# Kernel optimization log

Hardware: AMD Instinct MI355X
Metric: run time of the kernel (lower is better)

Reference implementation:

```python
import jax, jax.numpy as jnp
import numpy as np


def setup_inputs() -> dict:
    key = jax.random.key(0)
    ks = jax.random.split(key, 8)
    B, I, H, O, K = 4096, 512, 512, 512, 16
    s = 0.02
    return {
        "sample": jax.random.normal(ks[0], (B, I), jnp.float32),
        "hiddens": jax.random.normal(ks[1], (K, B, H), jnp.float32),
        "mem_para": jax.random.uniform(ks[2], (B, H), jnp.float32),
        "Wu": jax.random.normal(ks[3], (I + H, H), jnp.float32) * s,
        "bu": jnp.zeros((H,), jnp.float32),
        "Wr": jax.random.normal(ks[4], (I + H, H), jnp.float32) * s,
        "br": jnp.zeros((H,), jnp.float32),
        "Wm": jax.random.normal(ks[5], (I + 2 * H, H), jnp.float32) * s,
        "bm": jnp.zeros((H,), jnp.float32),
        "Wh": jax.random.normal(ks[6], (I + H, H), jnp.float32) * s,
        "bh": jnp.zeros((H,), jnp.float32),
        "Wo": jax.random.normal(ks[7], (H, O), jnp.float32) * s,
        "bo": jnp.zeros((O,), jnp.float32),
    }


def _mem_filter(hiddens, mem_para):
    # hiddens: [k, B, H]; mem_para (memory gate output, 'd'): [B, H]
    # Original per-scalar recurrence: w[k]=1; w[k-1-i] = w[k-i]*(i-d)/(i+1)
    # => w[k-1-i] = cumprod_{m=0..i} (m-d)/(m+1), i.e. signed fractional binomials.
    k = hiddens.shape[0]
    i = jnp.arange(k, dtype=hiddens.dtype)[:, None, None]          # [k,1,1]
    factors = (i - mem_para[None]) / (i + 1.0)                      # [k,B,H]
    weights = jnp.flip(jnp.cumprod(factors, axis=0), axis=0)        # [k,B,H]
    return jnp.sum(hiddens * weights, axis=0)                       # [B,H]


def reference(sample, hiddens, mem_para, Wu, bu, Wr, br, Wm, bm, Wh, bh, Wo, bo):
    hidden = hiddens[-1]                                            # [B,H]
    xh = jnp.concatenate([sample, hidden], axis=1)                  # [B,I+H]
    xhd = jnp.concatenate([xh, mem_para], axis=1)                   # [B,I+2H]
    update_gate = jax.nn.sigmoid(xh @ Wu + bu)
    reset_gate = jax.nn.sigmoid(xh @ Wr + br)
    memory_gate = 0.5 * jax.nn.sigmoid(xhd @ Wm + bm)
    xrh = jnp.concatenate([sample, reset_gate * hidden], axis=1)
    h_tilde = jnp.tanh(xrh @ Wh + bh)
    hiddens_filtered = -_mem_filter(hiddens, memory_gate)
    hidden_now = hiddens_filtered + update_gate * h_tilde           # [B,H]
    updated_hiddens = jnp.concatenate([hiddens[1:], hidden_now[None]], axis=0)
    output = hidden_now @ Wo + bo                                   # [B,O]
    return (output, updated_hiddens, memory_gate)
```

## Files before the change

### kernel.cpp

```cpp
#include <hip/hip_runtime.h>
#include <math.h>

typedef __bf16 bf16;
typedef __bf16 bf16x8 __attribute__((ext_vector_type(8)));
typedef __bf16 bf16x4 __attribute__((ext_vector_type(4)));
typedef float  f32x4  __attribute__((ext_vector_type(4)));

constexpr int BATCH = 4096;
constexpr int HID   = 512;
constexpr int NSTEP = 16;
constexpr int SLICE = BATCH * HID;
constexpr int S4    = SLICE / 4;

__device__ __forceinline__ float sigmoidf_(float x) {
    return 1.0f / (1.0f + __expf(-x));
}
__device__ __forceinline__ float tanh_fast(float x) {
    x = fminf(fmaxf(x, -15.0f), 15.0f);
    float e = __expf(2.0f * x);
    return (e - 1.0f) / (e + 1.0f);
}

__device__ __forceinline__ void gload_lds16(const void* g, void* l) {
    __builtin_amdgcn_global_load_lds((const __attribute__((address_space(1))) void*)g,
                                     (__attribute__((address_space(3))) void*)l,
                                     16, 0, 0);
}

__global__ __launch_bounds__(256)
void prep_all(const float* __restrict__ sample,
              const float* __restrict__ hidden,
              const float* __restrict__ mem_para,
              const float* __restrict__ Wu, const float* __restrict__ Wr,
              const float* __restrict__ Wm, const float* __restrict__ Wh,
              const float* __restrict__ Wo,
              bf16* __restrict__ Sb, bf16* __restrict__ Hb, bf16* __restrict__ Mb,
              bf16* __restrict__ Wall_t, bf16* __restrict__ Wh_t,
              bf16* __restrict__ Wo_t) {
    __shared__ float tile[32][33];
    const int bid = blockIdx.x;
    if (bid < 6144) {
        const int seg = bid >> 11;
        const int i = (bid & 2047) * 256 + threadIdx.x;
        const float* in = (seg == 0) ? sample : (seg == 1) ? hidden : mem_para;
        bf16* out = (seg == 0) ? Sb : (seg == 1) ? Hb : Mb;
        float4 v = ((const float4*)in)[i];
        bf16x4 o = {(bf16)v.x, (bf16)v.y, (bf16)v.z, (bf16)v.w};
        ((bf16x4*)out)[i] = o;
        return;
    }
    const int t = bid - 6144;
    const float* in; bf16* out; int stride, row_off, t2;
    if (t < 512)        { in = Wu; out = Wall_t; stride = 1536; row_off = 0;    t2 = t; }
    else if (t < 1024)  { in = Wr; out = Wall_t; stride = 1536; row_off = 512;  t2 = t - 512; }
    else if (t < 1792)  { in = Wm; out = Wall_t; stride = 1536; row_off = 1024; t2 = t - 1024; }
    else if (t < 2304)  { in = Wh; out = Wh_t;   stride = 1024; row_off = 0;    t2 = t - 1792; }
    else                { in = Wo; out = Wo_t;   stride = 512;  row_off = 0;    t2 = t - 2304; }
    const int r0 = (t2 >> 4) * 32, c0 = (t2 & 15) * 32;
    const int tr = threadIdx.x >> 5;
    const int tc = threadIdx.x & 31;
#pragma unroll
    for (int i = 0; i < 4; ++i)
        tile[tr + i * 8][tc] = in[(size_t)(r0 + tr + i * 8) * 512 + c0 + tc];
    __syncthreads();
#pragma unroll
    for (int i = 0; i < 4; ++i) {
        const int c = tr + i * 8;
        out[(size_t)(row_off + c0 + c) * stride + r0 + tc] = (bf16)tile[tc][c];
    }
}

__global__ __launch_bounds__(256)
void gemm_urm_copy(const bf16* __restrict__ Sb,
                   const bf16* __restrict__ Hb,
                   const bf16* __restrict__ Mb,
                   const bf16* __restrict__ Wall_t,
                   const float* __restrict__ bu,
                   const float* __restrict__ br,
                   const float* __restrict__ bm,
                   bf16* __restrict__ UGb,
                   bf16* __restrict__ RHb,
                   float* __restrict__ out_mg,
                   const float* __restrict__ hiddens,
                   float* __restrict__ out_upd) {
    __shared__ bf16 As[128 * 64];
    __shared__ bf16 Bs[64 * 64];

    const int bid = blockIdx.x;
    const int tid = threadIdx.x;

    if (bid >= 768) {
        const int base = (bid - 768) * 4096 + tid;
        const f32x4* src = ((const f32x4*)hiddens) + S4;
        f32x4* dst = (f32x4*)out_upd;
#pragma unroll
        for (int u = 0; u < 16; ++u) {
            const int f = base + u * 256;
            f32x4 v = __builtin_nontemporal_load(src + f);
            __builtin_nontemporal_store(v, dst + f);
        }
        return;
    }

    const int wid  = tid >> 6;
    const int lane = tid & 63;
    const int wr = wid >> 1, wc = wid & 1;
    const int brow = (bid & 31) * 128;
    const int bcol = (bid >> 5) * 64;

    const bf16* segs[3] = {Sb, Hb, Mb};
    const int nkt = (bcol >= 1024) ? 24 : 16;

    const int s_row  = tid >> 3;
    const int s_chnk = tid & 7;

    f32x4 acc[4][2] = {};

    for (int t = 0; t < nkt; ++t) {
        const int k0 = t * 64;
        const bf16* Aseg = segs[k0 >> 9];
        const int kloc = k0 & 511;

#pragma unroll
        for (int c = 0; c < 4; ++c) {
            const int row = c * 32 + s_row;
            const int sc  = s_chnk ^ (row & 7);
            gload_lds16(Aseg + (size_t)(brow + row) * 512 + kloc + sc * 8,
                        As + (size_t)(c * 256 + (wid << 6)) * 8);
        }
#pragma unroll
        for (int c = 0; c < 2; ++c) {
            const int row = c * 32 + s_row;
            const int sc  = s_chnk ^ (row & 7);
            gload_lds16(Wall_t + (size_t)(bcol + row) * 1536 + k0 + sc * 8,
                        Bs + (size_t)(c * 256 + (wid << 6)) * 8);
        }
        __syncthreads();

#pragma unroll
        for (int ks = 0; ks < 2; ++ks) {
            const int kb = ks * 64 + ((lane >> 4) << 4);
            bf16x8 bfrag[2];
#pragma unroll
            for (int ni = 0; ni < 2; ++ni) {
                const int n = wc * 32 + ni * 16 + (lane & 15);
                bfrag[ni] = *(const bf16x8*)((const char*)Bs +
                                             n * 128 + (kb ^ ((n & 7) << 4)));
            }
#pragma unroll
            for (int mi = 0; mi < 4; ++mi) {
                const int m = wr * 64 + mi * 16 + (lane & 15);
                const bf16x8 afrag = *(const bf16x8*)((const char*)As +
                                                      m * 128 + (kb ^ ((m & 7) << 4)));
#pragma unroll
                for (int ni = 0; ni < 2; ++ni)
                    acc[mi][ni] = __builtin_amdgcn_mfma_f32_16x16x32_bf16(
                        afrag, bfrag[ni], acc[mi][ni], 0, 0, 0);
            }
        }
        __syncthreads();
    }

    const int lr4 = (lane >> 4) * 4;
    const int lc  = lane & 15;
#pragma unroll
    for (int mi = 0; mi < 4; ++mi) {
#pragma unroll
        for (int ni = 0; ni < 2; ++ni) {
            const int col = bcol + wc * 32 + ni * 16 + lc;
            const f32x4 a = acc[mi][ni];
#pragma unroll
            for (int r = 0; r < 4; ++r) {
                const int row = brow + wr * 64 + mi * 16 + lr4 + r;
                const float x = a[r];
                if (col < 512) {
                    UGb[(size_t)row * 512 + col] = (bf16)sigmoidf_(x + bu[col]);
                } else if (col < 1024) {
                    const int c2 = col - 512;
                    const float v = sigmoidf_(x + br[c2]) *
                                    (float)Hb[(size_t)row * 512 + c2];
                    RHb[(size_t)row * 512 + c2] = (bf16)v;
                } else {
                    const int c3 = col - 1024;
                    out_mg[(size_t)row * 512 + c3] = 0.5f * sigmoidf_(x + bm[c3]);
                }
            }
        }
    }
}

__global__ __launch_bounds__(256)
void gemm_wh_sum(const bf16* __restrict__ Sb,
                 const bf16* __restrict__ RHb,
                 const bf16* __restrict__ Wh_t,
                 const float* __restrict__ bh,
                 bf16* __restrict__ HTb,
                 const float* __restrict__ hiddens,
                 const float* __restrict__ mg,
                 float* __restrict__ filt) {
    __shared__ bf16 As[128 * 64];
    __shared__ bf16 Bs[64 * 64];

    const int bid = blockIdx.x;
    const int tid = threadIdx.x;

    if (bid >= 256) {
        const int idx = (bid - 256) * 256 + tid;
        const f32x4 d = ((const f32x4*)mg)[idx];
        f32x4 c = {1.f, 1.f, 1.f, 1.f};
        f32x4 a = {0.f, 0.f, 0.f, 0.f};
#pragma unroll
        for (int i = 0; i < NSTEP; ++i) {
            const int j = NSTEP - 1 - i;
            const f32x4 v = __builtin_nontemporal_load(
                ((const f32x4*)hiddens) + (size_t)j * S4 + idx);
            const float fi = (float)i;
            const float inv = 1.0f / (float)(i + 1);
            c *= (fi - d) * inv;
            a += v * c;
        }
        __builtin_nontemporal_store(a, ((f32x4*)filt) + idx);
        return;
    }

    const int wid  = tid >> 6;
    const int lane = tid & 63;
    const int wr = wid >> 1, wc = wid & 1;
    const int brow = (bid & 31) * 128;
    const int bcol = (bid >> 5) * 64;

    const bf16* segs[2] = {Sb, RHb};

    const int s_row  = tid >> 3;
    const int s_chnk = tid & 7;

    f32x4 acc[4][2] = {};

    for (int t = 0; t < 16; ++t) {
        const int k0 = t * 64;
        const bf16* Aseg = segs[k0 >> 9];
        const int kloc = k0 & 511;

#pragma unroll
        for (int c = 0; c < 4; ++c) {
            const int row = c * 32 + s_row;
            const int sc  = s_chnk ^ (row & 7);
            gload_lds16(Aseg + (size_t)(brow + row) * 512 + kloc + sc * 8,
                        As + (size_t)(c * 256 + (wid << 6)) * 8);
        }
#pragma unroll
        for (int c = 0; c < 2; ++c) {
            const int row = c * 32 + s_row;
            const int sc  = s_chnk ^ (row & 7);
            gload_lds16(Wh_t + (size_t)(bcol + row) * 1024 + k0 + sc * 8,
                        Bs + (size_t)(c * 256 + (wid << 6)) * 8);
        }
        __syncthreads();

#pragma unroll
        for (int ks = 0; ks < 2; ++ks) {
            const int kb = ks * 64 + ((lane >> 4) << 4);
            bf16x8 bfrag[2];
#pragma unroll
            for (int ni = 0; ni < 2; ++ni) {
                const int n = wc * 32 + ni * 16 + (lane & 15);
                bfrag[ni] = *(const bf16x8*)((const char*)Bs +
                                             n * 128 + (kb ^ ((n & 7) << 4)));
            }
#pragma unroll
            for (int mi = 0; mi < 4; ++mi) {
                const int m = wr * 64 + mi * 16 + (lane & 15);
                const bf16x8 afrag = *(const bf16x8*)((const char*)As +
                                                      m * 128 + (kb ^ ((m & 7) << 4)));
#pragma unroll
                for (int ni = 0; ni < 2; ++ni)
                    acc[mi][ni] = __builtin_amdgcn_mfma_f32_16x16x32_bf16(
                        afrag, bfrag[ni], acc[mi][ni], 0, 0, 0);
            }
        }
        __syncthreads();
    }

    const int lr4 = (lane >> 4) * 4;
    const int lc  = lane & 15;
#pragma unroll
    for (int mi = 0; mi < 4; ++mi) {
#pragma unroll
        for (int ni = 0; ni < 2; ++ni) {
            const int col = bcol + wc * 32 + ni * 16 + lc;
            const f32x4 a = acc[mi][ni];
#pragma unroll
            for (int r = 0; r < 4; ++r) {
                const int row = brow + wr * 64 + mi * 16 + lr4 + r;
                HTb[(size_t)row * 512 + col] = (bf16)tanh_fast(a[r] + bh[col]);
            }
        }
    }
}

__global__ __launch_bounds__(256)
void combine(const float* __restrict__ filt,
             const bf16* __restrict__ ugb,
             const bf16* __restrict__ htb,
             float* __restrict__ out_upd,
             bf16* __restrict__ hnb) {
    const int idx = blockIdx.x * 256 + threadIdx.x;
    const f32x4 a = ((const f32x4*)filt)[idx];
    const bf16x4 u = ((const bf16x4*)ugb)[idx];
    const bf16x4 t = ((const bf16x4*)htb)[idx];
    f32x4 hn;
#pragma unroll
    for (int e = 0; e < 4; ++e)
        hn[e] = fmaf((float)u[e], (float)t[e], -a[e]);
    ((f32x4*)out_upd)[(size_t)(NSTEP - 1) * S4 + idx] = hn;
    bf16x4 hb = {(bf16)hn[0], (bf16)hn[1], (bf16)hn[2], (bf16)hn[3]};
    ((bf16x4*)hnb)[idx] = hb;
}

__global__ __launch_bounds__(256)
void gemm_out(const bf16* __restrict__ HNb,
              const bf16* __restrict__ Wo_t,
              const float* __restrict__ bo,
              float* __restrict__ outp) {
    __shared__ bf16 As[128 * 64];
    __shared__ bf16 Bs[64 * 64];

    const int tid  = threadIdx.x;
    const int wid  = tid >> 6;
    const int lane = tid & 63;
    const int wr = wid >> 1, wc = wid & 1;
    const int brow = blockIdx.x * 128;
    const int bcol = blockIdx.y * 64;

    const int s_row  = tid >> 3;
    const int s_chnk = tid & 7;

    f32x4 acc[4][2] = {};

    for (int t = 0; t < 8; ++t) {
        const int k0 = t * 64;

#pragma unroll
        for (int c = 0; c < 4; ++c) {
            const int row = c * 32 + s_row;
            const int sc  = s_chnk ^ (row & 7);
            gload_lds16(HNb + (size_t)(brow + row) * 512 + k0 + sc * 8,
                        As + (size_t)(c * 256 + (wid << 6)) * 8);
        }
#pragma unroll
        for (int c = 0; c < 2; ++c) {
            const int row = c * 32 + s_row;
            const int sc  = s_chnk ^ (row & 7);
            gload_lds16(Wo_t + (size_t)(bcol + row) * 512 + k0 + sc * 8,
                        Bs + (size_t)(c * 256 + (wid << 6)) * 8);
        }
        __syncthreads();

#pragma unroll
        for (int ks = 0; ks < 2; ++ks) {
            const int kb = ks * 64 + ((lane >> 4) << 4);
            bf16x8 bfrag[2];
#pragma unroll
            for (int ni = 0; ni < 2; ++ni) {
                const int n = wc * 32 + ni * 16 + (lane & 15);
                bfrag[ni] = *(const bf16x8*)((const char*)Bs +
                                             n * 128 + (kb ^ ((n & 7) << 4)));
            }
#pragma unroll
            for (int mi = 0; mi < 4; ++mi) {
                const int m = wr * 64 + mi * 16 + (lane & 15);
                const bf16x8 afrag = *(const bf16x8*)((const char*)As +
                                                      m * 128 + (kb ^ ((m & 7) << 4)));
#pragma unroll
                for (int ni = 0; ni < 2; ++ni)
                    acc[mi][ni] = __builtin_amdgcn_mfma_f32_16x16x32_bf16(
                        afrag, bfrag[ni], acc[mi][ni], 0, 0, 0);
            }
        }
        __syncthreads();
    }

    const int lr4 = (lane >> 4) * 4;
    const int lc  = lane & 15;
#pragma unroll
    for (int mi = 0; mi < 4; ++mi) {
#pragma unroll
        for (int ni = 0; ni < 2; ++ni) {
            const int col = bcol + wc * 32 + ni * 16 + lc;
            const f32x4 a = acc[mi][ni];
#pragma unroll
            for (int r = 0; r < 4; ++r) {
                const int row = brow + wr * 64 + mi * 16 + lr4 + r;
                outp[(size_t)row * 512 + col] = a[r] + bo[col];
            }
        }
    }
}

extern "C" void kernel_launch(void* const* d_in, const int* in_sizes, int n_in,
                              void* d_out, int out_size, void* d_ws, size_t ws_size,
                              hipStream_t stream) {
    const float* sample   = (const float*)d_in[0];
    const float* hiddens  = (const float*)d_in[1];
    const float* mem_para = (const float*)d_in[2];
    const float* Wu = (const float*)d_in[3];
    const float* bu = (const float*)d_in[4];
    const float* Wr = (const float*)d_in[5];
    const float* br = (const float*)d_in[6];
    const float* Wm = (const float*)d_in[7];
    const float* bm = (const float*)d_in[8];
    const float* Wh = (const float*)d_in[9];
    const float* bh = (const float*)d_in[10];
    const float* Wo = (const float*)d_in[11];
    const float* bo = (const float*)d_in[12];

    float* out        = (float*)d_out;
    float* out_output = out;
    float* out_upd    = out + SLICE;
    float* out_mg     = out + SLICE + (size_t)NSTEP * SLICE;

    const float* hidden = hiddens + (size_t)(NSTEP - 1) * SLICE;

    char* ws = (char*)d_ws;
    bf16* Sb    = (bf16*)(ws);
    bf16* Hb    = (bf16*)(ws + (((size_t) 4) << 20));
    bf16* Mb    = (bf16*)(ws + (((size_t) 8) << 20));
    bf16* RHb   = (bf16*)(ws + (((size_t)12) << 20));
    bf16* HNb   = (bf16*)(ws + (((size_t)16) << 20));
    bf16* UGb   = (bf16*)(ws + (((size_t)20) << 20));
    bf16* HTb   = (bf16*)(ws + (((size_t)24) << 20));
    bf16* Wall_t = (bf16*)(ws + (((size_t)28) << 20));
    bf16* Wh_t  = (bf16*)(ws + (((size_t)33) << 20));
    bf16* Wo_t  = (bf16*)(ws + (((size_t)35) << 20));
    float* filt = (float*)(ws + (((size_t)40) << 20));

    dim3 blk(256);

    prep_all<<<8704, blk, 0, stream>>>(sample, hidden, mem_para,
                                       Wu, Wr, Wm, Wh, Wo,
                                       Sb, Hb, Mb, Wall_t, Wh_t, Wo_t);
    gemm_urm_copy<<<768 + 1920, blk, 0, stream>>>(
        Sb, Hb, Mb, Wall_t, bu, br, bm, UGb, RHb, out_mg, hiddens, out_upd);
    gemm_wh_sum<<<256 + 2048, blk, 0, stream>>>(
        Sb, RHb, Wh_t, bh, HTb, hiddens, out_mg, filt);
    combine<<<S4 / 256, blk, 0, stream>>>(filt, UGb, HTb, out_upd, HNb);
    gemm_out<<<dim3(32, 8), blk, 0, stream>>>(HNb, Wo_t, bo, out_output);
}
```

Measured before the change: 130.5 us.

## Fuse hiddens shift-copy into filter pass and remap GEMM blocks across XCDs

The separate copy of hiddens[1:] into updated_hiddens is removed from the first GEMM launch. It is now done inside the memory-filter pass, which already reads every hiddens slice, so each slice is read once instead of twice. All three GEMMs also use a new block-index mapping that groups row blocks per XCD (bid&7), with the aim of improving L2 reuse of the A and B tiles. The filter pass switches its loads from nontemporal to normal loads and now issues more stores, which may lengthen that phase.

```diff
diff --git a/kernel.cpp b/kernel.cpp
--- a/kernel.cpp
+++ b/kernel.cpp
@@ -71,45 +71,35 @@
 }
 
 __global__ __launch_bounds__(256)
-void gemm_urm_copy(const bf16* __restrict__ Sb,
-                   const bf16* __restrict__ Hb,
-                   const bf16* __restrict__ Mb,
-                   const bf16* __restrict__ Wall_t,
-                   const float* __restrict__ bu,
-                   const float* __restrict__ br,
-                   const float* __restrict__ bm,
-                   bf16* __restrict__ UGb,
-                   bf16* __restrict__ RHb,
-                   float* __restrict__ out_mg,
-                   const float* __restrict__ hiddens,
-                   float* __restrict__ out_upd) {
+void gemm_urm(const bf16* __restrict__ Sb,
+              const bf16* __restrict__ Hb,
+              const bf16* __restrict__ Mb,
+              const bf16* __restrict__ Wall_t,
+              const float* __restrict__ bu,
+              const float* __restrict__ br,
+              const float* __restrict__ bm,
+              bf16* __restrict__ UGb,
+              bf16* __restrict__ RHb,
+              float* __restrict__ out_mg) {
     __shared__ bf16 As[128 * 64];
     __shared__ bf16 Bs[64 * 64];
 
     const int bid = blockIdx.x;
     const int tid = threadIdx.x;
 
-    if (bid >= 768) {
-        const int base = (bid - 768) * 4096 + tid;
-        const f32x4* src = ((const f32x4*)hiddens) + S4;
-        f32x4* dst = (f32x4*)out_upd;
-#pragma unroll
-        for (int u = 0; u < 16; ++u) {
-            const int f = base + u * 256;
-            f32x4 v = __builtin_nontemporal_load(src + f);
-            __builtin_nontemporal_store(v, dst + f);
-        }
-        return;
-    }
+    const int k8  = bid & 7;
+    const int s   = bid >> 3;
+    const int colb = s >> 2;
+    const int rowb = (k8 << 2) + (s & 3);
+    const int brow = rowb * 128;
+    const int bcol = colb * 64;
 
     const int wid  = tid >> 6;
     const int lane = tid & 63;
     const int wr = wid >> 1, wc = wid & 1;
-    const int brow = (bid & 31) * 128;
-    const int bcol = (bid >> 5) * 64;
 
     const bf16* segs[3] = {Sb, Hb, Mb};
-    const int nkt = (bcol >= 1024) ? 24 : 16;
+    const int nkt = (colb >= 16) ? 24 : 16;
 
     const int s_row  = tid >> 3;
     const int s_chnk = tid & 7;
@@ -190,14 +180,15 @@
 }
 
 __global__ __launch_bounds__(256)
-void gemm_wh_sum(const bf16* __restrict__ Sb,
-                 const bf16* __restrict__ RHb,
-                 const bf16* __restrict__ Wh_t,
-                 const float* __restrict__ bh,
-                 bf16* __restrict__ HTb,
-                 const float* __restrict__ hiddens,
-                 const float* __restrict__ mg,
-                 float* __restrict__ filt) {
+void gemm_wh_filter(const bf16* __restrict__ Sb,
+                    const bf16* __restrict__ RHb,
+                    const bf16* __restrict__ Wh_t,
+                    const float* __restrict__ bh,
+                    bf16* __restrict__ HTb,
+                    const float* __restrict__ hiddens,
+                    const float* __restrict__ mg,
+                    float* __restrict__ out_upd,
+                    float* __restrict__ filt) {
     __shared__ bf16 As[128 * 64];
     __shared__ bf16 Bs[64 * 64];
 
@@ -206,28 +197,36 @@
 
     if (bid >= 256) {
         const int idx = (bid - 256) * 256 + tid;
+        const f32x4* h4 = (const f32x4*)hiddens;
+        f32x4* o4 = (f32x4*)out_upd;
         const f32x4 d = ((const f32x4*)mg)[idx];
         f32x4 c = {1.f, 1.f, 1.f, 1.f};
         f32x4 a = {0.f, 0.f, 0.f, 0.f};
 #pragma unroll
         for (int i = 0; i < NSTEP; ++i) {
             const int j = NSTEP - 1 - i;
-            const f32x4 v = __builtin_nontemporal_load(
-                ((const f32x4*)hiddens) + (size_t)j * S4 + idx);
+            const f32x4 v = h4[(size_t)j * S4 + idx];
             const float fi = (float)i;
             const float inv = 1.0f / (float)(i + 1);
             c *= (fi - d) * inv;
             a += v * c;
-        }
-        __builtin_nontemporal_store(a, ((f32x4*)filt) + idx);
+            if (j >= 1)
+                __builtin_nontemporal_store(v, o4 + (size_t)(j - 1) * S4 + idx);
+        }
+        ((f32x4*)filt)[idx] = a;
         return;
     }
+
+    const int k8  = bid & 7;
+    const int s   = bid >> 3;
+    const int colb = s >> 2;
+    const int rowb = (k8 << 2) + (s & 3);
+    const int brow = rowb * 128;
+    const int bcol = colb * 64;
 
     const int wid  = tid >> 6;
     const int lane = tid & 63;
     const int wr = wid >> 1, wc = wid & 1;
-    const int brow = (bid & 31) * 128;
-    const int bcol = (bid >> 5) * 64;
 
     const bf16* segs[2] = {Sb, RHb};
 
@@ -325,12 +324,19 @@
     __shared__ bf16 As[128 * 64];
     __shared__ bf16 Bs[64 * 64];
 
-    const int tid  = threadIdx.x;
+    const int bid = blockIdx.x;
+    const int tid = threadIdx.x;
+
+    const int k8  = bid & 7;
+    const int s   = bid >> 3;
+    const int colb = s >> 2;
+    const int rowb = (k8 << 2) + (s & 3);
+    const int brow = rowb * 128;
+    const int bcol = colb * 64;
+
     const int wid  = tid >> 6;
     const int lane = tid & 63;
     const int wr = wid >> 1, wc = wid & 1;
-    const int brow = blockIdx.x * 128;
-    const int bcol = blockIdx.y * 64;
 
     const int s_row  = tid >> 3;
     const int s_chnk = tid & 7;
@@ -439,10 +445,10 @@
     prep_all<<<8704, blk, 0, stream>>>(sample, hidden, mem_para,
                                        Wu, Wr, Wm, Wh, Wo,
                                        Sb, Hb, Mb, Wall_t, Wh_t, Wo_t);
-    gemm_urm_copy<<<768 + 1920, blk, 0, stream>>>(
-        Sb, Hb, Mb, Wall_t, bu, br, bm, UGb, RHb, out_mg, hiddens, out_upd);
-    gemm_wh_sum<<<256 + 2048, blk, 0, stream>>>(
-        Sb, RHb, Wh_t, bh, HTb, hiddens, out_mg, filt);
+    gemm_urm<<<768, blk, 0, stream>>>(
+        Sb, Hb, Mb, Wall_t, bu, br, bm, UGb, RHb, out_mg);
+    gemm_wh_filter<<<256 + 2048, blk, 0, stream>>>(
+        Sb, RHb, Wh_t, bh, HTb, hiddens, out_mg, out_upd, filt);
     combine<<<S4 / 256, blk, 0, stream>>>(filt, UGb, HTb, out_upd, HNb);
-    gemm_out<<<dim3(32, 8), blk, 0, stream>>>(HNb, Wo_t, bo, out_output);
-}
+    gemm_out<<<256, blk, 0, stream>>>(HNb, Wo_t, bo, out_output);
+}
```

Measured after the change: 107.8 us. -17.4%, faster.
